# Kernel optimization log

Measured on AMD Instinct MI355X. Metric: run time of the kernel, lower is better.

Reference implementation:

```python
import jax, jax.numpy as jnp
import numpy as np

N_NODES = 200000   # total graph nodes (var + constraint)
N_VAR   = 112000   # nodes with x[:,0]==1, placed first for static slicing
N_EDGES = 3200000  # avg degree 16
HID     = 64
BATCH   = 64       # fc output width == batch_size in the torch module
TW      = 8        # target_width; TW*(TW-1)=56; N_VAR = seq_len*56 with seq_len=2000


def setup_inputs() -> dict:
    key = jax.random.key(0)
    ks = jax.random.split(key, 8)
    x = jax.random.normal(ks[0], (N_NODES, 2), jnp.float32)
    # var_mask = (x[:,0] == 1): make the first N_VAR nodes variable nodes.
    x = x.at[:, 0].set(jnp.where(jnp.arange(N_NODES) < N_VAR, 1.0, 0.0))
    edge_index = jax.random.randint(ks[1], (2, N_EDGES), 0, N_NODES, jnp.int32)
    W1 = jax.random.normal(ks[2], (2, HID), jnp.float32) / np.sqrt(2.0)
    b1 = jnp.zeros((HID,), jnp.float32)
    W2 = jax.random.normal(ks[3], (HID, HID), jnp.float32) / np.sqrt(HID)
    b2 = jnp.zeros((HID,), jnp.float32)
    Wfc = jax.random.normal(ks[4], (HID, BATCH), jnp.float32) / np.sqrt(HID)
    bfc = jnp.zeros((BATCH,), jnp.float32)
    return {"x": x, "edge_index": edge_index, "W1": W1, "b1": b1,
            "W2": W2, "b2": b2, "Wfc": Wfc, "bfc": bfc}


def gcn_conv(x, src, dst, W, b):
    """PyG GCNConv: transform, then sym-normalized aggregation with self-loops."""
    h = x @ W                                   # [N, F_out]
    ones = jnp.ones(src.shape[0], x.dtype)
    deg = jax.ops.segment_sum(ones, dst, num_segments=N_NODES) + 1.0  # +1: self-loop
    dinv = jax.lax.rsqrt(deg)                   # deg >= 1, always safe
    norm = dinv[src] * dinv[dst]                # [E]
    agg = jax.ops.segment_sum(h[src] * norm[:, None], dst, num_segments=N_NODES)
    agg = agg + h * (dinv * dinv)[:, None]      # self-loop message, norm = dinv_i^2
    return agg + b


def reference(x, edge_index, W1, b1, W2, b2, Wfc, bfc):
    src, dst = edge_index[0], edge_index[1]
    h = jax.nn.relu(gcn_conv(x, src, dst, W1, b1))
    h = gcn_conv(h, src, dst, W2, b2)
    # var_mask == first N_VAR rows by construction (static slice for jit)
    out = jax.nn.relu(h[:N_VAR] @ Wfc + bfc)    # [N_VAR, BATCH]
    width = TW * (TW - 1)                       # 56
    seq_len = N_VAR // width                    # 2000
    return jnp.round(out.reshape(seq_len, BATCH, width))
```

## Files before the change

### kernel.cpp

```cpp
#include <hip/hip_runtime.h>
#include <math.h>

#define N_NODES 200000
#define N_VAR   112000
#define N_EDGES 3200000
#define NB_SCAN 782
#define CAP     64

#define NFINE    512
#define PSZ_F    391
#define FCAP     7168
#define BIN_CHUNK 8192
#define NB_BIN   391

typedef int v4i __attribute__((ext_vector_type(4)));

__device__ __forceinline__ float bcast_lane(float x, int lane) {
    return __int_as_float(__builtin_amdgcn_readlane(__float_as_int(x), lane));
}

__global__ void __launch_bounds__(256) k_setup(const float* __restrict__ W2,
                                               const float* __restrict__ b2,
                                               const float* __restrict__ Wfc,
                                               const float* __restrict__ bfc,
                                               float* __restrict__ Wc,
                                               float* __restrict__ bc,
                                               int* __restrict__ bcnt) {
    int b = blockIdx.x;
    int i = b * 256 + threadIdx.x;
    if (i < NFINE) bcnt[i] = 0;
    if (b < 16) {
        int e = b * 256 + threadIdx.x;
        int j = e >> 6, l = e & 63;
        double acc = 0.0;
        for (int m = 0; m < 64; ++m)
            acc += (double)W2[j * 64 + m] * (double)Wfc[m * 64 + l];
        Wc[e] = (float)acc;
    } else if (b == 16 && threadIdx.x < 64) {
        int l = threadIdx.x;
        double acc = (double)bfc[l];
        for (int m = 0; m < 64; ++m)
            acc += (double)b2[m] * (double)Wfc[m * 64 + l];
        bc[l] = (float)acc;
    }
}

__global__ void __launch_bounds__(512) k_bin(const int* __restrict__ src,
                                             const int* __restrict__ dst,
                                             int* __restrict__ bins,
                                             int* __restrict__ bcnt) {
    __shared__ int hist[NFINE];
    __shared__ int seg[NFINE];
    __shared__ int gb[NFINE];
    __shared__ int cur[NFINE];
    __shared__ int scn[NFINE];
    __shared__ int stg[BIN_CHUNK];
    __shared__ unsigned short stgb[BIN_CHUNK];
    int tid = threadIdx.x;
    hist[tid] = 0;
    __syncthreads();

    int base = blockIdx.x * BIN_CHUNK;
    int pk[4][4];
    int bk[4][4];
    bool val[4];
    #pragma unroll
    for (int i = 0; i < 4; ++i) {
        int e4 = base + (i * 512 + tid) * 4;
        val[i] = (e4 < N_EDGES);
        if (val[i]) {
            v4i d = __builtin_nontemporal_load((const v4i*)(dst + e4));
            v4i s = __builtin_nontemporal_load((const v4i*)(src + e4));
            int dd[4] = {d.x, d.y, d.z, d.w};
            int ss[4] = {s.x, s.y, s.z, s.w};
            #pragma unroll
            for (int q = 0; q < 4; ++q) {
                int bb = dd[q] / PSZ_F;
                int dl = dd[q] - bb * PSZ_F;
                pk[i][q] = (dl << 18) | ss[q];
                bk[i][q] = bb;
                atomicAdd(&hist[bb], 1);
            }
        }
    }
    __syncthreads();

    scn[tid] = hist[tid];
    __syncthreads();
    for (int d = 1; d < NFINE; d <<= 1) {
        int t = scn[tid];
        int u = (tid >= d) ? scn[tid - d] : 0;
        __syncthreads();
        scn[tid] = t + u;
        __syncthreads();
    }
    int ex = scn[tid] - hist[tid];
    seg[tid] = ex;
    cur[tid] = ex;
    gb[tid]  = atomicAdd(&bcnt[tid], hist[tid]);
    __syncthreads();
    int tot = scn[NFINE - 1];

    #pragma unroll
    for (int i = 0; i < 4; ++i) {
        if (val[i]) {
            #pragma unroll
            for (int q = 0; q < 4; ++q) {
                int p = atomicAdd(&cur[bk[i][q]], 1);
                stg[p]  = pk[i][q];
                stgb[p] = (unsigned short)bk[i][q];
            }
        }
    }
    __syncthreads();

    for (int i = tid; i < tot; i += 512) {
        int bb  = stgb[i];
        int pos = gb[bb] + (i - seg[bb]);
        if (pos < FCAP)
            bins[(size_t)bb * FCAP + pos] = stg[i];
    }
}

__global__ void __launch_bounds__(512) k_sort(const int* __restrict__ bins,
                                              const int* __restrict__ bcnt,
                                              int* __restrict__ cnt,
                                              int* __restrict__ buf) {
    __shared__ int hist[NFINE];
    __shared__ int scn[NFINE];
    __shared__ int off[NFINE];
    __shared__ int cur[NFINE];
    __shared__ int sorted[FCAP];
    __shared__ unsigned short rowid[FCAP];
    int tid = threadIdx.x;
    int b = blockIdx.x;
    int n = bcnt[b];
    if (n > FCAP) n = FCAP;
    const int* __restrict__ bp = bins + (size_t)b * FCAP;

    hist[tid] = 0;
    __syncthreads();
    for (int i = tid; i < n; i += 512)
        atomicAdd(&hist[bp[i] >> 18], 1);
    __syncthreads();

    int v = b * PSZ_F + tid;
    if (tid < PSZ_F && v < N_NODES) cnt[v] = hist[tid];

    scn[tid] = hist[tid];
    __syncthreads();
    for (int d = 1; d < NFINE; d <<= 1) {
        int t = scn[tid];
        int u = (tid >= d) ? scn[tid - d] : 0;
        __syncthreads();
        scn[tid] = t + u;
        __syncthreads();
    }
    int ex = scn[tid] - hist[tid];
    off[tid] = ex;
    cur[tid] = ex;
    __syncthreads();

    for (int i = tid; i < n; i += 512) {
        int pk = bp[i];
        int dl = pk >> 18;
        int p = atomicAdd(&cur[dl], 1);
        sorted[p] = pk & 0x3FFFF;
        rowid[p]  = (unsigned short)dl;
    }
    __syncthreads();

    for (int i = tid; i < n; i += 512) {
        int dl = rowid[i];
        int slot = i - off[dl];
        if (slot < CAP)
            buf[(size_t)(b * PSZ_F + dl) * CAP + slot] = sorted[i];
    }
}

__global__ void __launch_bounds__(256) k_post(const int* __restrict__ cnt,
                                              const float2* __restrict__ x2,
                                              float4* __restrict__ xdc) {
    int i = blockIdx.x * 256 + threadIdx.x;
    if (i >= N_NODES) return;
    float dv = rsqrtf((float)cnt[i] + 1.0f);
    float2 xv = x2[i];
    xdc[i] = make_float4(xv.x * dv, xv.y * dv, dv, 0.0f);
}

__global__ void __launch_bounds__(256) k_l1a(const int* __restrict__ cnt,
                                             const int* __restrict__ buf,
                                             const float4* __restrict__ xdc,
                                             float4* __restrict__ zn) {
    int v = blockIdx.x * 256 + threadIdx.x;
    if (v >= N_NODES) return;
    int c = cnt[v];
    int n = (c < CAP) ? c : CAP;
    const int* __restrict__ rowp = buf + v * CAP;
    float4 self = xdc[v];
    float dv = self.z;
    float ax = self.x, ay = self.y;
    float bx = 0.0f,   by = 0.0f;
    int j = 0;
    for (; j + 16 <= n; j += 16) {
        v4i r0 = *(const v4i*)(rowp + j);
        v4i r1 = *(const v4i*)(rowp + j + 4);
        v4i r2 = *(const v4i*)(rowp + j + 8);
        v4i r3 = *(const v4i*)(rowp + j + 12);
        float4 p0 = xdc[r0.x], p1 = xdc[r0.y], p2 = xdc[r0.z], p3 = xdc[r0.w];
        float4 p4 = xdc[r1.x], p5 = xdc[r1.y], p6 = xdc[r1.z], p7 = xdc[r1.w];
        float4 p8 = xdc[r2.x], p9 = xdc[r2.y], pa = xdc[r2.z], pb = xdc[r2.w];
        float4 pc = xdc[r3.x], pd = xdc[r3.y], pe = xdc[r3.z], pf = xdc[r3.w];
        ax += p0.x; ay += p0.y;  bx += p1.x; by += p1.y;
        ax += p2.x; ay += p2.y;  bx += p3.x; by += p3.y;
        ax += p4.x; ay += p4.y;  bx += p5.x; by += p5.y;
        ax += p6.x; ay += p6.y;  bx += p7.x; by += p7.y;
        ax += p8.x; ay += p8.y;  bx += p9.x; by += p9.y;
        ax += pa.x; ay += pa.y;  bx += pb.x; by += pb.y;
        ax += pc.x; ay += pc.y;  bx += pd.x; by += pd.y;
        ax += pe.x; ay += pe.y;  bx += pf.x; by += pf.y;
    }
    for (; j + 8 <= n; j += 8) {
        v4i r0 = *(const v4i*)(rowp + j);
        v4i r1 = *(const v4i*)(rowp + j + 4);
        float4 p0 = xdc[r0.x], p1 = xdc[r0.y], p2 = xdc[r0.z], p3 = xdc[r0.w];
        float4 p4 = xdc[r1.x], p5 = xdc[r1.y], p6 = xdc[r1.z], p7 = xdc[r1.w];
        ax += p0.x; ay += p0.y;  bx += p1.x; by += p1.y;
        ax += p2.x; ay += p2.y;  bx += p3.x; by += p3.y;
        ax += p4.x; ay += p4.y;  bx += p5.x; by += p5.y;
        ax += p6.x; ay += p6.y;  bx += p7.x; by += p7.y;
    }
    for (; j < n; ++j) {
        int s = rowp[j];
        float4 p = xdc[s];
        ax += p.x; ay += p.y;
    }
    zn[v] = make_float4((ax + bx) * dv, (ay + by) * dv, dv, 0.0f);
}

__global__ void __launch_bounds__(256, 4) k_l2(const int* __restrict__ cnt,
                                               const int* __restrict__ buf,
                                               const float4* __restrict__ zn,
                                               const float* __restrict__ W1,
                                               const float* __restrict__ b1,
                                               const float* __restrict__ Wc,
                                               const float* __restrict__ bc,
                                               float* __restrict__ out) {
    int w = threadIdx.x >> 6, l = threadIdx.x & 63;
    float wc[64];
    #pragma unroll
    for (int jv = 0; jv < 64; ++jv)
        wc[jv] = Wc[jv * 64 + l];
    float w1a = W1[l], w1b = W1[64 + l], bb = b1[l];
    float bcl = bc[l];
    int v0 = blockIdx.x * 16 + w;
    int cA = __builtin_amdgcn_readfirstlane(cnt[v0]);
    int cB = __builtin_amdgcn_readfirstlane(cnt[v0 + 4]);
    int cC = __builtin_amdgcn_readfirstlane(cnt[v0 + 8]);
    int cD = __builtin_amdgcn_readfirstlane(cnt[v0 + 12]);

    #pragma unroll
    for (int it = 0; it < 4; ++it) {
        int v = v0 + it * 4;
        int c = (it == 0) ? cA : (it == 1) ? cB : (it == 2) ? cC : cD;
        int n = (c < CAP) ? c : CAP;
        float dv = rsqrtf((float)c + 1.0f);
        const int* __restrict__ row = buf + v * CAP;

        int ridx = row[l];
        int idx  = (l < n) ? ridx : v;
        float4 p = zn[idx];

        float4 zs = zn[v];
        float acc0 = fmaxf(fmaf(zs.x, w1a, fmaf(zs.y, w1b, bb)), 0.0f) * zs.z;
        float acc1 = 0.0f;
        int j = 0;
        for (; j + 8 <= n; j += 8) {
            float x0 = bcast_lane(p.x, j+0), y0 = bcast_lane(p.y, j+0), z0 = bcast_lane(p.z, j+0);
            float x1 = bcast_lane(p.x, j+1), y1 = bcast_lane(p.y, j+1), z1 = bcast_lane(p.z, j+1);
            float x2 = bcast_lane(p.x, j+2), y2 = bcast_lane(p.y, j+2), z2 = bcast_lane(p.z, j+2);
            float x3 = bcast_lane(p.x, j+3), y3 = bcast_lane(p.y, j+3), z3 = bcast_lane(p.z, j+3);
            float x4 = bcast_lane(p.x, j+4), y4 = bcast_lane(p.y, j+4), z4 = bcast_lane(p.z, j+4);
            float x5 = bcast_lane(p.x, j+5), y5 = bcast_lane(p.y, j+5), z5 = bcast_lane(p.z, j+5);
            float x6 = bcast_lane(p.x, j+6), y6 = bcast_lane(p.y, j+6), z6 = bcast_lane(p.z, j+6);
            float x7 = bcast_lane(p.x, j+7), y7 = bcast_lane(p.y, j+7), z7 = bcast_lane(p.z, j+7);
            float h0 = fmaxf(fmaf(x0, w1a, fmaf(y0, w1b, bb)), 0.0f) * z0;
            float h1 = fmaxf(fmaf(x1, w1a, fmaf(y1, w1b, bb)), 0.0f) * z1;
            float h2 = fmaxf(fmaf(x2, w1a, fmaf(y2, w1b, bb)), 0.0f) * z2;
            float h3 = fmaxf(fmaf(x3, w1a, fmaf(y3, w1b, bb)), 0.0f) * z3;
            float h4 = fmaxf(fmaf(x4, w1a, fmaf(y4, w1b, bb)), 0.0f) * z4;
            float h5 = fmaxf(fmaf(x5, w1a, fmaf(y5, w1b, bb)), 0.0f) * z5;
            float h6 = fmaxf(fmaf(x6, w1a, fmaf(y6, w1b, bb)), 0.0f) * z6;
            float h7 = fmaxf(fmaf(x7, w1a, fmaf(y7, w1b, bb)), 0.0f) * z7;
            acc0 += (h0 + h1) + (h2 + h3);
            acc1 += (h4 + h5) + (h6 + h7);
        }
        for (; j + 4 <= n; j += 4) {
            float x0 = bcast_lane(p.x, j+0), y0 = bcast_lane(p.y, j+0), z0 = bcast_lane(p.z, j+0);
            float x1 = bcast_lane(p.x, j+1), y1 = bcast_lane(p.y, j+1), z1 = bcast_lane(p.z, j+1);
            float x2 = bcast_lane(p.x, j+2), y2 = bcast_lane(p.y, j+2), z2 = bcast_lane(p.z, j+2);
            float x3 = bcast_lane(p.x, j+3), y3 = bcast_lane(p.y, j+3), z3 = bcast_lane(p.z, j+3);
            float h0 = fmaxf(fmaf(x0, w1a, fmaf(y0, w1b, bb)), 0.0f) * z0;
            float h1 = fmaxf(fmaf(x1, w1a, fmaf(y1, w1b, bb)), 0.0f) * z1;
            float h2 = fmaxf(fmaf(x2, w1a, fmaf(y2, w1b, bb)), 0.0f) * z2;
            float h3 = fmaxf(fmaf(x3, w1a, fmaf(y3, w1b, bb)), 0.0f) * z3;
            acc0 += (h0 + h1) + (h2 + h3);
        }
        for (; j < n; ++j) {
            float xk = bcast_lane(p.x, j), yk = bcast_lane(p.y, j), zk = bcast_lane(p.z, j);
            acc1 += fmaxf(fmaf(xk, w1a, fmaf(yk, w1b, bb)), 0.0f) * zk;
        }
        float Av = (acc0 + acc1) * dv;

        float t0 = 0.0f, t1 = 0.0f, t2 = 0.0f, t3 = 0.0f;
        #pragma unroll
        for (int jj = 0; jj < 64; jj += 4) {
            t0 = fmaf(bcast_lane(Av, jj + 0), wc[jj + 0], t0);
            t1 = fmaf(bcast_lane(Av, jj + 1), wc[jj + 1], t1);
            t2 = fmaf(bcast_lane(Av, jj + 2), wc[jj + 2], t2);
            t3 = fmaf(bcast_lane(Av, jj + 3), wc[jj + 3], t3);
        }
        float t = ((t0 + t1) + (t2 + t3)) + bcl;
        out[v * 64 + l] = rintf(fmaxf(t, 0.0f));
    }
}


extern "C" void kernel_launch(void* const* d_in, const int* in_sizes, int n_in,
                              void* d_out, int out_size, void* d_ws, size_t ws_size,
                              hipStream_t stream) {
    const float* x    = (const float*)d_in[0];
    const int*   ei   = (const int*)  d_in[1];
    const float* W1   = (const float*)d_in[2];
    const float* b1   = (const float*)d_in[3];
    const float* W2   = (const float*)d_in[4];
    const float* b2   = (const float*)d_in[5];
    const float* Wfc  = (const float*)d_in[6];
    const float* bfc  = (const float*)d_in[7];
    float* out = (float*)d_out;

    const int* src = ei;
    const int* dst = ei + N_EDGES;

    char* ws = (char*)d_ws;
    int*    cnt    = (int*)   (ws + 0);
    float4* xdc    = (float4*)(ws + 3204096);
    float4* zn     = (float4*)(ws + 6404096);
    int*    bins   = (int*)   (ws + 3204096);
    int*    bcnt   = (int*)   (ws + 17884160);
    int*    buf    = (int*)   (ws + 19204096);
    float*  Wc     = (float*) (ws + 70404096);
    float*  bc     = (float*) (ws + 70420480);

    k_setup <<<NB_SCAN, 256, 0, stream>>>(W2, b2, Wfc, bfc, Wc, bc, bcnt);
    k_bin   <<<NB_BIN, 512, 0, stream>>>(src, dst, bins, bcnt);
    k_sort  <<<NFINE, 512, 0, stream>>>(bins, bcnt, cnt, buf);
    k_post  <<<NB_SCAN, 256, 0, stream>>>(cnt, (const float2*)x, xdc);
    k_l1a   <<<NB_SCAN, 256, 0, stream>>>(cnt, buf, xdc, zn);
    k_l2    <<<N_VAR / 16, 256, 0, stream>>>(cnt, buf, zn, W1, b1, Wc, bc, out);
}
```

Measured before the change: 218.3 us.

## Fuse setup and post kernels into bin/sort, use wave-shuffle scans, tune binning

Removes the k_setup and k_post launches. The weight-product computation moves into k_bin, the degree/normalization step moves into k_sort, and bcnt is zeroed with a memset instead. The block-wide shared-memory Hillis-Steele scans are replaced with wavefront shuffle scans plus per-wave sums, which cuts the number of barriers. Binning chunks are halved and the block count doubled for more parallelism. k_l2 now issues all four gather loads up front, and nontemporal loads and stores are added for the neighbor lists and the output. The workspace layout is repacked, which risks overlaps between buffers.

```diff
diff --git a/kernel.cpp b/kernel.cpp
--- a/kernel.cpp
+++ b/kernel.cpp
@@ -10,62 +10,43 @@
 #define NFINE    512
 #define PSZ_F    391
 #define FCAP     7168
-#define BIN_CHUNK 8192
-#define NB_BIN   391
+#define BIN_CHUNK 4096
+#define NB_BIN   782
 
 typedef int v4i __attribute__((ext_vector_type(4)));
 
 __device__ __forceinline__ float bcast_lane(float x, int lane) {
     return __int_as_float(__builtin_amdgcn_readlane(__float_as_int(x), lane));
-}
-
-__global__ void __launch_bounds__(256) k_setup(const float* __restrict__ W2,
-                                               const float* __restrict__ b2,
-                                               const float* __restrict__ Wfc,
-                                               const float* __restrict__ bfc,
-                                               float* __restrict__ Wc,
-                                               float* __restrict__ bc,
-                                               int* __restrict__ bcnt) {
-    int b = blockIdx.x;
-    int i = b * 256 + threadIdx.x;
-    if (i < NFINE) bcnt[i] = 0;
-    if (b < 16) {
-        int e = b * 256 + threadIdx.x;
-        int j = e >> 6, l = e & 63;
-        double acc = 0.0;
-        for (int m = 0; m < 64; ++m)
-            acc += (double)W2[j * 64 + m] * (double)Wfc[m * 64 + l];
-        Wc[e] = (float)acc;
-    } else if (b == 16 && threadIdx.x < 64) {
-        int l = threadIdx.x;
-        double acc = (double)bfc[l];
-        for (int m = 0; m < 64; ++m)
-            acc += (double)b2[m] * (double)Wfc[m * 64 + l];
-        bc[l] = (float)acc;
-    }
 }
 
 __global__ void __launch_bounds__(512) k_bin(const int* __restrict__ src,
                                              const int* __restrict__ dst,
                                              int* __restrict__ bins,
-                                             int* __restrict__ bcnt) {
+                                             int* __restrict__ bcnt,
+                                             const float* __restrict__ W2,
+                                             const float* __restrict__ b2,
+                                             const float* __restrict__ Wfc,
+                                             const float* __restrict__ bfc,
+                                             float* __restrict__ Wc,
+                                             float* __restrict__ bc) {
     __shared__ int hist[NFINE];
     __shared__ int seg[NFINE];
     __shared__ int gb[NFINE];
     __shared__ int cur[NFINE];
-    __shared__ int scn[NFINE];
+    __shared__ int wsum[8];
     __shared__ int stg[BIN_CHUNK];
     __shared__ unsigned short stgb[BIN_CHUNK];
     int tid = threadIdx.x;
+    int lane = tid & 63, wid = tid >> 6;
     hist[tid] = 0;
     __syncthreads();
 
     int base = blockIdx.x * BIN_CHUNK;
-    int pk[4][4];
-    int bk[4][4];
-    bool val[4];
-    #pragma unroll
-    for (int i = 0; i < 4; ++i) {
+    int pk[2][4];
+    int bk[2][4];
+    bool val[2];
+    #pragma unroll
+    for (int i = 0; i < 2; ++i) {
         int e4 = base + (i * 512 + tid) * 4;
         val[i] = (e4 < N_EDGES);
         if (val[i]) {
@@ -75,34 +56,40 @@
             int ss[4] = {s.x, s.y, s.z, s.w};
             #pragma unroll
             for (int q = 0; q < 4; ++q) {
-                int bb = dd[q] / PSZ_F;
-                int dl = dd[q] - bb * PSZ_F;
+                int bb2 = dd[q] / PSZ_F;
+                int dl = dd[q] - bb2 * PSZ_F;
                 pk[i][q] = (dl << 18) | ss[q];
-                bk[i][q] = bb;
-                atomicAdd(&hist[bb], 1);
+                bk[i][q] = bb2;
+                atomicAdd(&hist[bb2], 1);
             }
         }
     }
     __syncthreads();
 
-    scn[tid] = hist[tid];
-    __syncthreads();
-    for (int d = 1; d < NFINE; d <<= 1) {
-        int t = scn[tid];
-        int u = (tid >= d) ? scn[tid - d] : 0;
-        __syncthreads();
-        scn[tid] = t + u;
-        __syncthreads();
-    }
-    int ex = scn[tid] - hist[tid];
+    int h = hist[tid];
+    int inc = h;
+    #pragma unroll
+    for (int d = 1; d < 64; d <<= 1) {
+        int t = __shfl_up(inc, d);
+        if (lane >= d) inc += t;
+    }
+    if (lane == 63) wsum[wid] = inc;
+    __syncthreads();
+    int pre = 0, tot = 0;
+    #pragma unroll
+    for (int k = 0; k < 8; ++k) {
+        int s = wsum[k];
+        pre += (k < wid) ? s : 0;
+        tot += s;
+    }
+    int ex = pre + inc - h;
     seg[tid] = ex;
     cur[tid] = ex;
-    gb[tid]  = atomicAdd(&bcnt[tid], hist[tid]);
-    __syncthreads();
-    int tot = scn[NFINE - 1];
-
-    #pragma unroll
-    for (int i = 0; i < 4; ++i) {
+    gb[tid]  = atomicAdd(&bcnt[tid], h);
+    __syncthreads();
+
+    #pragma unroll
+    for (int i = 0; i < 2; ++i) {
         if (val[i]) {
             #pragma unroll
             for (int q = 0; q < 4; ++q) {
@@ -115,24 +102,42 @@
     __syncthreads();
 
     for (int i = tid; i < tot; i += 512) {
-        int bb  = stgb[i];
-        int pos = gb[bb] + (i - seg[bb]);
+        int bb2 = stgb[i];
+        int pos = gb[bb2] + (i - seg[bb2]);
         if (pos < FCAP)
-            bins[(size_t)bb * FCAP + pos] = stg[i];
+            bins[(size_t)bb2 * FCAP + pos] = stg[i];
+    }
+
+    int b = blockIdx.x;
+    if (b < 8) {
+        int e = b * 512 + tid;
+        int j = e >> 6, l2 = e & 63;
+        double acc = 0.0;
+        for (int m = 0; m < 64; ++m)
+            acc += (double)W2[j * 64 + m] * (double)Wfc[m * 64 + l2];
+        Wc[e] = (float)acc;
+    } else if (b == 8 && tid < 64) {
+        double acc = (double)bfc[tid];
+        for (int m = 0; m < 64; ++m)
+            acc += (double)b2[m] * (double)Wfc[m * 64 + tid];
+        bc[tid] = (float)acc;
     }
 }
 
 __global__ void __launch_bounds__(512) k_sort(const int* __restrict__ bins,
                                               const int* __restrict__ bcnt,
+                                              const float2* __restrict__ x2,
                                               int* __restrict__ cnt,
+                                              float4* __restrict__ xdc,
                                               int* __restrict__ buf) {
     __shared__ int hist[NFINE];
-    __shared__ int scn[NFINE];
     __shared__ int off[NFINE];
     __shared__ int cur[NFINE];
+    __shared__ int wsum[8];
     __shared__ int sorted[FCAP];
     __shared__ unsigned short rowid[FCAP];
     int tid = threadIdx.x;
+    int lane = tid & 63, wid = tid >> 6;
     int b = blockIdx.x;
     int n = bcnt[b];
     if (n > FCAP) n = FCAP;
@@ -144,28 +149,40 @@
         atomicAdd(&hist[bp[i] >> 18], 1);
     __syncthreads();
 
-    int v = b * PSZ_F + tid;
-    if (tid < PSZ_F && v < N_NODES) cnt[v] = hist[tid];
-
-    scn[tid] = hist[tid];
-    __syncthreads();
-    for (int d = 1; d < NFINE; d <<= 1) {
-        int t = scn[tid];
-        int u = (tid >= d) ? scn[tid - d] : 0;
-        __syncthreads();
-        scn[tid] = t + u;
-        __syncthreads();
-    }
-    int ex = scn[tid] - hist[tid];
+    int h = hist[tid];
+
+    int vg = b * PSZ_F + tid;
+    if (tid < PSZ_F && vg < N_NODES) {
+        cnt[vg] = h;
+        float dvv = rsqrtf((float)h + 1.0f);
+        float2 xv = x2[vg];
+        xdc[vg] = make_float4(xv.x * dvv, xv.y * dvv, dvv, 0.0f);
+    }
+
+    int inc = h;
+    #pragma unroll
+    for (int d = 1; d < 64; d <<= 1) {
+        int t = __shfl_up(inc, d);
+        if (lane >= d) inc += t;
+    }
+    if (lane == 63) wsum[wid] = inc;
+    __syncthreads();
+    int pre = 0;
+    #pragma unroll
+    for (int k = 0; k < 8; ++k) {
+        int s = wsum[k];
+        pre += (k < wid) ? s : 0;
+    }
+    int ex = pre + inc - h;
     off[tid] = ex;
     cur[tid] = ex;
     __syncthreads();
 
     for (int i = tid; i < n; i += 512) {
-        int pk = bp[i];
-        int dl = pk >> 18;
+        int pkv = bp[i];
+        int dl = pkv >> 18;
         int p = atomicAdd(&cur[dl], 1);
-        sorted[p] = pk & 0x3FFFF;
+        sorted[p] = pkv & 0x3FFFF;
         rowid[p]  = (unsigned short)dl;
     }
     __syncthreads();
@@ -176,16 +193,6 @@
         if (slot < CAP)
             buf[(size_t)(b * PSZ_F + dl) * CAP + slot] = sorted[i];
     }
-}
-
-__global__ void __launch_bounds__(256) k_post(const int* __restrict__ cnt,
-                                              const float2* __restrict__ x2,
-                                              float4* __restrict__ xdc) {
-    int i = blockIdx.x * 256 + threadIdx.x;
-    if (i >= N_NODES) return;
-    float dv = rsqrtf((float)cnt[i] + 1.0f);
-    float2 xv = x2[i];
-    xdc[i] = make_float4(xv.x * dv, xv.y * dv, dv, 0.0f);
 }
 
 __global__ void __launch_bounds__(256) k_l1a(const int* __restrict__ cnt,
@@ -203,10 +210,10 @@
     float bx = 0.0f,   by = 0.0f;
     int j = 0;
     for (; j + 16 <= n; j += 16) {
-        v4i r0 = *(const v4i*)(rowp + j);
-        v4i r1 = *(const v4i*)(rowp + j + 4);
-        v4i r2 = *(const v4i*)(rowp + j + 8);
-        v4i r3 = *(const v4i*)(rowp + j + 12);
+        v4i r0 = __builtin_nontemporal_load((const v4i*)(rowp + j));
+        v4i r1 = __builtin_nontemporal_load((const v4i*)(rowp + j + 4));
+        v4i r2 = __builtin_nontemporal_load((const v4i*)(rowp + j + 8));
+        v4i r3 = __builtin_nontemporal_load((const v4i*)(rowp + j + 12));
         float4 p0 = xdc[r0.x], p1 = xdc[r0.y], p2 = xdc[r0.z], p3 = xdc[r0.w];
         float4 p4 = xdc[r1.x], p5 = xdc[r1.y], p6 = xdc[r1.z], p7 = xdc[r1.w];
         float4 p8 = xdc[r2.x], p9 = xdc[r2.y], pa = xdc[r2.z], pb = xdc[r2.w];
@@ -221,8 +228,8 @@
         ax += pe.x; ay += pe.y;  bx += pf.x; by += pf.y;
     }
     for (; j + 8 <= n; j += 8) {
-        v4i r0 = *(const v4i*)(rowp + j);
-        v4i r1 = *(const v4i*)(rowp + j + 4);
+        v4i r0 = __builtin_nontemporal_load((const v4i*)(rowp + j));
+        v4i r1 = __builtin_nontemporal_load((const v4i*)(rowp + j + 4));
         float4 p0 = xdc[r0.x], p1 = xdc[r0.y], p2 = xdc[r0.z], p3 = xdc[r0.w];
         float4 p4 = xdc[r1.x], p5 = xdc[r1.y], p6 = xdc[r1.z], p7 = xdc[r1.w];
         ax += p0.x; ay += p0.y;  bx += p1.x; by += p1.y;
@@ -254,36 +261,46 @@
     float w1a = W1[l], w1b = W1[64 + l], bb = b1[l];
     float bcl = bc[l];
     int v0 = blockIdx.x * 16 + w;
-    int cA = __builtin_amdgcn_readfirstlane(cnt[v0]);
-    int cB = __builtin_amdgcn_readfirstlane(cnt[v0 + 4]);
-    int cC = __builtin_amdgcn_readfirstlane(cnt[v0 + 8]);
-    int cD = __builtin_amdgcn_readfirstlane(cnt[v0 + 12]);
-
+    int cc0 = __builtin_amdgcn_readfirstlane(cnt[v0]);
+    int cc1 = __builtin_amdgcn_readfirstlane(cnt[v0 + 4]);
+    int cc2 = __builtin_amdgcn_readfirstlane(cnt[v0 + 8]);
+    int cc3 = __builtin_amdgcn_readfirstlane(cnt[v0 + 12]);
+
+    int nn[4];
+    float4 p[4], zs[4];
     #pragma unroll
     for (int it = 0; it < 4; ++it) {
         int v = v0 + it * 4;
-        int c = (it == 0) ? cA : (it == 1) ? cB : (it == 2) ? cC : cD;
+        int c = (it == 0) ? cc0 : (it == 1) ? cc1 : (it == 2) ? cc2 : cc3;
         int n = (c < CAP) ? c : CAP;
+        nn[it] = n;
+        int ridx = __builtin_nontemporal_load(buf + v * CAP + l);
+        int idx  = (l < n) ? ridx : v;
+        p[it]  = zn[idx];
+        zs[it] = zn[v];
+    }
+
+    #pragma unroll
+    for (int it = 0; it < 4; ++it) {
+        int v = v0 + it * 4;
+        int c = (it == 0) ? cc0 : (it == 1) ? cc1 : (it == 2) ? cc2 : cc3;
+        int n = nn[it];
         float dv = rsqrtf((float)c + 1.0f);
-        const int* __restrict__ row = buf + v * CAP;
-
-        int ridx = row[l];
-        int idx  = (l < n) ? ridx : v;
-        float4 p = zn[idx];
-
-        float4 zs = zn[v];
-        float acc0 = fmaxf(fmaf(zs.x, w1a, fmaf(zs.y, w1b, bb)), 0.0f) * zs.z;
+        float4 pp = p[it];
+        float4 zss = zs[it];
+
+        float acc0 = fmaxf(fmaf(zss.x, w1a, fmaf(zss.y, w1b, bb)), 0.0f) * zss.z;
         float acc1 = 0.0f;
         int j = 0;
         for (; j + 8 <= n; j += 8) {
-            float x0 = bcast_lane(p.x, j+0), y0 = bcast_lane(p.y, j+0), z0 = bcast_lane(p.z, j+0);
-            float x1 = bcast_lane(p.x, j+1), y1 = bcast_lane(p.y, j+1), z1 = bcast_lane(p.z, j+1);
-            float x2 = bcast_lane(p.x, j+2), y2 = bcast_lane(p.y, j+2), z2 = bcast_lane(p.z, j+2);
-            float x3 = bcast_lane(p.x, j+3), y3 = bcast_lane(p.y, j+3), z3 = bcast_lane(p.z, j+3);
-            float x4 = bcast_lane(p.x, j+4), y4 = bcast_lane(p.y, j+4), z4 = bcast_lane(p.z, j+4);
-            float x5 = bcast_lane(p.x, j+5), y5 = bcast_lane(p.y, j+5), z5 = bcast_lane(p.z, j+5);
-            float x6 = bcast_lane(p.x, j+6), y6 = bcast_lane(p.y, j+6), z6 = bcast_lane(p.z, j+6);
-            float x7 = bcast_lane(p.x, j+7), y7 = bcast_lane(p.y, j+7), z7 = bcast_lane(p.z, j+7);
+            float x0 = bcast_lane(pp.x, j+0), y0 = bcast_lane(pp.y, j+0), z0 = bcast_lane(pp.z, j+0);
+            float x1 = bcast_lane(pp.x, j+1), y1 = bcast_lane(pp.y, j+1), z1 = bcast_lane(pp.z, j+1);
+            float x2 = bcast_lane(pp.x, j+2), y2 = bcast_lane(pp.y, j+2), z2 = bcast_lane(pp.z, j+2);
+            float x3 = bcast_lane(pp.x, j+3), y3 = bcast_lane(pp.y, j+3), z3 = bcast_lane(pp.z, j+3);
+            float x4 = bcast_lane(pp.x, j+4), y4 = bcast_lane(pp.y, j+4), z4 = bcast_lane(pp.z, j+4);
+            float x5 = bcast_lane(pp.x, j+5), y5 = bcast_lane(pp.y, j+5), z5 = bcast_lane(pp.z, j+5);
+            float x6 = bcast_lane(pp.x, j+6), y6 = bcast_lane(pp.y, j+6), z6 = bcast_lane(pp.z, j+6);
+            float x7 = bcast_lane(pp.x, j+7), y7 = bcast_lane(pp.y, j+7), z7 = bcast_lane(pp.z, j+7);
             float h0 = fmaxf(fmaf(x0, w1a, fmaf(y0, w1b, bb)), 0.0f) * z0;
             float h1 = fmaxf(fmaf(x1, w1a, fmaf(y1, w1b, bb)), 0.0f) * z1;
             float h2 = fmaxf(fmaf(x2, w1a, fmaf(y2, w1b, bb)), 0.0f) * z2;
@@ -296,10 +313,10 @@
             acc1 += (h4 + h5) + (h6 + h7);
         }
         for (; j + 4 <= n; j += 4) {
-            float x0 = bcast_lane(p.x, j+0), y0 = bcast_lane(p.y, j+0), z0 = bcast_lane(p.z, j+0);
-            float x1 = bcast_lane(p.x, j+1), y1 = bcast_lane(p.y, j+1), z1 = bcast_lane(p.z, j+1);
-            float x2 = bcast_lane(p.x, j+2), y2 = bcast_lane(p.y, j+2), z2 = bcast_lane(p.z, j+2);
-            float x3 = bcast_lane(p.x, j+3), y3 = bcast_lane(p.y, j+3), z3 = bcast_lane(p.z, j+3);
+            float x0 = bcast_lane(pp.x, j+0), y0 = bcast_lane(pp.y, j+0), z0 = bcast_lane(pp.z, j+0);
+            float x1 = bcast_lane(pp.x, j+1), y1 = bcast_lane(pp.y, j+1), z1 = bcast_lane(pp.z, j+1);
+            float x2 = bcast_lane(pp.x, j+2), y2 = bcast_lane(pp.y, j+2), z2 = bcast_lane(pp.z, j+2);
+            float x3 = bcast_lane(pp.x, j+3), y3 = bcast_lane(pp.y, j+3), z3 = bcast_lane(pp.z, j+3);
             float h0 = fmaxf(fmaf(x0, w1a, fmaf(y0, w1b, bb)), 0.0f) * z0;
             float h1 = fmaxf(fmaf(x1, w1a, fmaf(y1, w1b, bb)), 0.0f) * z1;
             float h2 = fmaxf(fmaf(x2, w1a, fmaf(y2, w1b, bb)), 0.0f) * z2;
@@ -307,7 +324,7 @@
             acc0 += (h0 + h1) + (h2 + h3);
         }
         for (; j < n; ++j) {
-            float xk = bcast_lane(p.x, j), yk = bcast_lane(p.y, j), zk = bcast_lane(p.z, j);
+            float xk = bcast_lane(pp.x, j), yk = bcast_lane(pp.y, j), zk = bcast_lane(pp.z, j);
             acc1 += fmaxf(fmaf(xk, w1a, fmaf(yk, w1b, bb)), 0.0f) * zk;
         }
         float Av = (acc0 + acc1) * dv;
@@ -321,7 +338,7 @@
             t3 = fmaf(bcast_lane(Av, jj + 3), wc[jj + 3], t3);
         }
         float t = ((t0 + t1) + (t2 + t3)) + bcl;
-        out[v * 64 + l] = rintf(fmaxf(t, 0.0f));
+        __builtin_nontemporal_store(rintf(fmaxf(t, 0.0f)), out + v * 64 + l);
     }
 }
 
@@ -344,18 +361,17 @@
 
     char* ws = (char*)d_ws;
     int*    cnt    = (int*)   (ws + 0);
-    float4* xdc    = (float4*)(ws + 3204096);
-    float4* zn     = (float4*)(ws + 6404096);
-    int*    bins   = (int*)   (ws + 3204096);
-    int*    bcnt   = (int*)   (ws + 17884160);
+    float4* xdc    = (float4*)(ws + 800000);
+    int*    bins   = (int*)   (ws + 4000000);
+    int*    bcnt   = (int*)   (ws + 18680064);
+    float4* zn     = (float4*)(ws + 15204096);
     int*    buf    = (int*)   (ws + 19204096);
     float*  Wc     = (float*) (ws + 70404096);
     float*  bc     = (float*) (ws + 70420480);
 
-    k_setup <<<NB_SCAN, 256, 0, stream>>>(W2, b2, Wfc, bfc, Wc, bc, bcnt);
-    k_bin   <<<NB_BIN, 512, 0, stream>>>(src, dst, bins, bcnt);
-    k_sort  <<<NFINE, 512, 0, stream>>>(bins, bcnt, cnt, buf);
-    k_post  <<<NB_SCAN, 256, 0, stream>>>(cnt, (const float2*)x, xdc);
-    k_l1a   <<<NB_SCAN, 256, 0, stream>>>(cnt, buf, xdc, zn);
-    k_l2    <<<N_VAR / 16, 256, 0, stream>>>(cnt, buf, zn, W1, b1, Wc, bc, out);
-}
+    hipMemsetAsync(bcnt, 0, NFINE * sizeof(int), stream);
+    k_bin  <<<NB_BIN, 512, 0, stream>>>(src, dst, bins, bcnt, W2, b2, Wfc, bfc, Wc, bc);
+    k_sort <<<NFINE, 512, 0, stream>>>(bins, bcnt, (const float2*)x, cnt, xdc, buf);
+    k_l1a  <<<NB_SCAN, 256, 0, stream>>>(cnt, buf, xdc, zn);
+    k_l2   <<<N_VAR / 16, 256, 0, stream>>>(cnt, buf, zn, W1, b1, Wc, bc, out);
+}
```

After: 225.4 us. +3.3%, slower.
